# Kernel optimization log

Measured on AMD Instinct MI355X. Metric: run time of the kernel, lower is better.

Reference implementation:

```python
import jax, jax.numpy as jnp
import numpy as np

DIM = 1024
NUM_HEADS = 16
HEAD_DIM = DIM // NUM_HEADS
HIDDEN = 4 * DIM
EPS = 1e-5


def rmsnorm(x, w):
    var = jnp.mean(jnp.square(x), axis=-1, keepdims=True)
    return x * jax.lax.rsqrt(var + EPS) * w


def setup_inputs() -> dict:
    key = jax.random.key(0)
    ks = jax.random.split(key, 10)
    s = 0.02
    return {
        "x": jax.random.normal(ks[0], (2, 2048, DIM), dtype=jnp.float32),
        "wq": jax.random.normal(ks[1], (DIM, DIM), dtype=jnp.float32) * s,
        "wk": jax.random.normal(ks[2], (DIM, DIM), dtype=jnp.float32) * s,
        "wv": jax.random.normal(ks[3], (DIM, DIM), dtype=jnp.float32) * s,
        "wo": jax.random.normal(ks[4], (DIM, DIM), dtype=jnp.float32) * s,
        "wgate": jax.random.normal(ks[5], (HIDDEN, DIM), dtype=jnp.float32) * s,
        "wup": jax.random.normal(ks[6], (HIDDEN, DIM), dtype=jnp.float32) * s,
        "wdown": jax.random.normal(ks[7], (DIM, HIDDEN), dtype=jnp.float32) * s,
        "norm1_w": jnp.ones((DIM,), dtype=jnp.float32),
        "norm2_w": jnp.ones((DIM,), dtype=jnp.float32),
    }


def reference(x, wq, wk, wv, wo, wgate, wup, wdown, norm1_w, norm2_w):
    B, S, _ = x.shape
    residual = x
    h = rmsnorm(x, norm1_w)
    # torch Linear: y = x @ W.T  (W is [out, in])
    q = (h @ wq.T).reshape(B, S, NUM_HEADS, HEAD_DIM)
    k = (h @ wk.T).reshape(B, S, NUM_HEADS, HEAD_DIM)
    v = (h @ wv.T).reshape(B, S, NUM_HEADS, HEAD_DIM)
    scale = HEAD_DIM ** -0.5
    # [B, H, S, S] scores, causal mask
    scores = jnp.einsum("bqhd,bkhd->bhqk", q, k) * scale
    causal = jnp.tril(jnp.ones((S, S), dtype=bool))
    scores = jnp.where(causal, scores, -jnp.inf)
    attn = jax.nn.softmax(scores, axis=-1)
    out = jnp.einsum("bhqk,bkhd->bqhd", attn, v).reshape(B, S, DIM)
    x = residual + out @ wo.T
    residual = x
    h = rmsnorm(x, norm2_w)
    mlp = (jax.nn.silu(h @ wgate.T) * (h @ wup.T)) @ wdown.T
    return residual + mlp
```

## Files before the change

### kernel.cpp

```cpp
#include <hip/hip_runtime.h>
#include <stdint.h>

typedef __attribute__((ext_vector_type(4))) float  f32x4;
typedef __attribute__((ext_vector_type(8))) __bf16 bf16x8;
typedef __attribute__((ext_vector_type(4))) unsigned short us4;

__device__ __forceinline__ unsigned short f2bf(float f) {
  unsigned int u = __float_as_uint(f);
  unsigned int r = (u + 0x7fffu + ((u >> 16) & 1u)) >> 16;
  return (unsigned short)r;
}
__device__ __forceinline__ float bf2f(unsigned short h) {
  return __uint_as_float(((unsigned int)h) << 16);
}
__device__ __forceinline__ void gload16(const void* g, void* l) {
  __builtin_amdgcn_global_load_lds((const __attribute__((address_space(1))) void*)g,
                                   (__attribute__((address_space(3))) void*)l, 16, 0, 0);
}

__global__ __launch_bounds__(256) void convert_w(
    const float* __restrict__ wq, const float* __restrict__ wk, const float* __restrict__ wv,
    const float* __restrict__ wo, const float* __restrict__ wg, const float* __restrict__ wu,
    const float* __restrict__ wd, unsigned short* __restrict__ dst)
{
  long vid = (long)blockIdx.x * 256 + threadIdx.x;
  long e = vid * 4;
  const float* s; long base;
  if (e < (1L << 22)) { int wi = (int)(e >> 20); s = wi == 0 ? wq : wi == 1 ? wk : wi == 2 ? wv : wo; base = (long)wi << 20; }
  else if (e < (2L << 22)) { s = wg; base = 1L << 22; }
  else if (e < (3L << 22)) { s = wu; base = 2L << 22; }
  else                     { s = wd; base = 3L << 22; }
  f32x4 v = *(const f32x4*)(s + (e - base));
  us4 o; o.x = f2bf(v.x); o.y = f2bf(v.y); o.z = f2bf(v.z); o.w = f2bf(v.w);
  *(us4*)(dst + e) = o;
}

__global__ __launch_bounds__(256) void rmsnorm_k(const float* __restrict__ x,
                                                 const float* __restrict__ w,
                                                 unsigned short* __restrict__ h)
{
  const int row = blockIdx.x, t = threadIdx.x;
  const float* xr = x + (long)row * 1024;
  f32x4 v = *(const f32x4*)(xr + t * 4);
  float ss = v.x * v.x + v.y * v.y + v.z * v.z + v.w * v.w;
  #pragma unroll
  for (int o = 32; o > 0; o >>= 1) ss += __shfl_xor(ss, o);
  __shared__ float red[4];
  if ((t & 63) == 0) red[t >> 6] = ss;
  __syncthreads();
  ss = red[0] + red[1] + red[2] + red[3];
  float sc = rsqrtf(ss * (1.0f / 1024.0f) + 1e-5f);
  f32x4 wv = *(const f32x4*)(w + t * 4);
  us4 o4;
  o4.x = f2bf(v.x * sc * wv.x);
  o4.y = f2bf(v.y * sc * wv.y);
  o4.z = f2bf(v.z * sc * wv.z);
  o4.w = f2bf(v.w * sc * wv.w);
  *(us4*)(h + (long)row * 1024 + t * 4) = o4;
}

template<int EPI, int BM>
__global__ __launch_bounds__(256) void gemm_bt(
    const unsigned short* __restrict__ A, const unsigned short* __restrict__ B,
    int M, int N, int K, void* __restrict__ out0,
    const float* __restrict__ resid, const unsigned short* __restrict__ gbuf)
{
  constexpr int MI = (BM == 128) ? 4 : 2;
  __shared__ __align__(16) unsigned short Al[BM * 64];
  __shared__ __align__(16) unsigned short Bl[128 * 64];
  const int t = threadIdx.x;
  const int lane = t & 63;
  const int wid = t >> 6;
  const int wr = wid >> 1, wc = wid & 1;
  const long m0 = (long)blockIdx.x * BM;
  const long n0 = (long)blockIdx.y * 128;
  const int lr = lane & 15, lk = (lane >> 4) * 8;
  f32x4 acc[MI][4] = {};
  const int trow = t >> 3, tcol = (t & 7) * 8;
  const unsigned short* Ag = A + (m0 + trow) * (long)K + tcol;
  const unsigned short* Bg = B + (n0 + trow) * (long)K + tcol;
  unsigned short* Ald = Al + trow * 64 + tcol;
  unsigned short* Bld = Bl + trow * 64 + tcol;
  const int nkt = K >> 6;
  for (int kt = 0; kt < nkt; ++kt) {
    #pragma unroll
    for (int i = 0; i < BM / 32; ++i)
      gload16(Ag + (long)kt * 64 + (long)i * 32 * K, Ald + i * 2048);
    #pragma unroll
    for (int i = 0; i < 4; ++i)
      gload16(Bg + (long)kt * 64 + (long)i * 32 * K, Bld + i * 2048);
    __syncthreads();
    #pragma unroll
    for (int kk = 0; kk < 64; kk += 32) {
      bf16x8 af[MI], bfr[4];
      #pragma unroll
      for (int mi = 0; mi < MI; ++mi)
        af[mi] = *(const bf16x8*)&Al[(wr * (MI * 16) + mi * 16 + lr) * 64 + kk + lk];
      #pragma unroll
      for (int ni = 0; ni < 4; ++ni)
        bfr[ni] = *(const bf16x8*)&Bl[(wc * 64 + ni * 16 + lr) * 64 + kk + lk];
      #pragma unroll
      for (int mi = 0; mi < MI; ++mi)
        #pragma unroll
        for (int ni = 0; ni < 4; ++ni)
          acc[mi][ni] = __builtin_amdgcn_mfma_f32_16x16x32_bf16(af[mi], bfr[ni], acc[mi][ni], 0, 0, 0);
    }
    __syncthreads();
  }
  const int lg = lane >> 4;
  #pragma unroll
  for (int mi = 0; mi < MI; ++mi)
    #pragma unroll
    for (int ni = 0; ni < 4; ++ni)
      #pragma unroll
      for (int j = 0; j < 4; ++j) {
        long row = m0 + wr * (MI * 16) + mi * 16 + lg * 4 + j;
        long col = n0 + wc * 64 + ni * 16 + lr;
        float v = acc[mi][ni][j];
        if (EPI == 0) {
          unsigned short* qkv = (unsigned short*)out0;
          long b = row >> 11, s = row & 2047;
          if (col < 1024) {
            long hh = col >> 6, d = col & 63;
            qkv[((b * 16 + hh) * 2048 + s) * 64 + d] = f2bf(v);
          } else if (col < 2048) {
            long c = col - 1024, hh = c >> 6, d = c & 63;
            qkv[4194304 + ((b * 16 + hh) * 2048 + s) * 64 + d] = f2bf(v);
          } else {
            long c = col - 2048, hh = c >> 6, d = c & 63;
            qkv[8388608 + ((b * 16 + hh) * 64 + d) * 2048 + s] = f2bf(v);
          }
        } else if (EPI == 1) {
          ((float*)out0)[row * N + col] = resid[row * N + col] + v;
        }
      }
}

template<int EPI>
__global__ __launch_bounds__(512, 2) void gemm8(
    const unsigned short* __restrict__ A, const unsigned short* __restrict__ B,
    int M, int N, int K, unsigned short* __restrict__ out0,
    const unsigned short* __restrict__ gbuf)
{
  __shared__ __align__(16) unsigned short Asl[2][2][8192];
  __shared__ __align__(16) unsigned short Bsl[2][2][8192];
  const int t = threadIdx.x;
  const int lane = t & 63, w = t >> 6;
  const int wr = w >> 2, wc = w & 3;
  const int lr = lane & 15, lg = lane >> 4;
  const int nwg = gridDim.x * gridDim.y;
  int lid = blockIdx.y * gridDim.x + blockIdx.x;
  if ((nwg & 7) == 0) lid = (lid & 7) * (nwg >> 3) + (lid >> 3);
  const long m0 = (long)(lid % gridDim.x) * 256;
  const long n0 = (long)(lid / gridDim.x) * 256;

  const int swb = ((lr >> 2) & 1) << 5;
  const int colx0 = (lg * 16) ^ swb;
  const int colx1 = (64 + lg * 16) ^ swb;

  const int scol = ((t & 7) * 8) ^ (((t >> 5) & 1) << 4);
  const int srow = t >> 3;

  auto stage = [&](int kt, int buf) {
    const long kc = (long)kt * 64 + scol;
    #pragma unroll
    for (int h = 0; h < 2; ++h)
      #pragma unroll
      for (int j = 0; j < 2; ++j) {
        const int row = h * 128 + j * 64 + srow;
        gload16(&A[(m0 + row) * (long)K + kc], &Asl[buf][h][j * 4096 + t * 8]);
        gload16(&B[(n0 + row) * (long)K + kc], &Bsl[buf][h][j * 4096 + t * 8]);
      }
  };

  f32x4 acc[8][4] = {};
  const int nkt = K >> 6;

  stage(0, 0);
  __syncthreads();

  for (int kt = 0; kt < nkt; ++kt) {
    const int p = kt & 1;
    const char* Ab = (const char*)Asl[p][wr];
    const char* Bb = (const char*)Bsl[p][wc >> 1];
    bf16x8 breg[4][2];
    #pragma unroll
    for (int ni = 0; ni < 4; ++ni) {
      const int brow = (wc & 1) * 64 + ni * 16 + lr;
      breg[ni][0] = *(const bf16x8*)(Bb + brow * 128 + colx0);
      breg[ni][1] = *(const bf16x8*)(Bb + brow * 128 + colx1);
    }
    #pragma unroll
    for (int q2 = 0; q2 < 4; ++q2) {
      bf16x8 areg[2][2];
      #pragma unroll
      for (int mi = 0; mi < 2; ++mi) {
        const int arow = q2 * 32 + mi * 16 + lr;
        areg[mi][0] = *(const bf16x8*)(Ab + arow * 128 + colx0);
        areg[mi][1] = *(const bf16x8*)(Ab + arow * 128 + colx1);
      }
      if (q2 == 0 && kt + 1 < nkt) stage(kt + 1, p ^ 1);
      __builtin_amdgcn_s_setprio(1);
      #pragma unroll
      for (int mi = 0; mi < 2; ++mi)
        #pragma unroll
        for (int ni = 0; ni < 4; ++ni) {
          acc[q2 * 2 + mi][ni] = __builtin_amdgcn_mfma_f32_16x16x32_bf16(
              areg[mi][0], breg[ni][0], acc[q2 * 2 + mi][ni], 0, 0, 0);
          acc[q2 * 2 + mi][ni] = __builtin_amdgcn_mfma_f32_16x16x32_bf16(
              areg[mi][1], breg[ni][1], acc[q2 * 2 + mi][ni], 0, 0, 0);
        }
      __builtin_amdgcn_s_setprio(0);
      if (q2 < 3) __builtin_amdgcn_s_barrier();
    }
    asm volatile("s_waitcnt vmcnt(0)" ::: "memory");
    __builtin_amdgcn_s_barrier();
    __builtin_amdgcn_sched_barrier(0);
  }

  #pragma unroll
  for (int fi = 0; fi < 8; ++fi)
    #pragma unroll
    for (int ni = 0; ni < 4; ++ni)
      #pragma unroll
      for (int j = 0; j < 4; ++j) {
        long row = m0 + wr * 128 + fi * 16 + lg * 4 + j;
        long col = n0 + wc * 64 + ni * 16 + lr;
        float v = acc[fi][ni][j];
        if (EPI == 2) {
          out0[row * N + col] = f2bf(v);
        } else {
          float g = bf2f(gbuf[row * N + col]);
          float sg = g / (1.0f + __expf(-g));
          out0[row * N + col] = f2bf(sg * v);
        }
      }
}

__global__ __launch_bounds__(256) void attn_k(
    const unsigned short* __restrict__ qb, const unsigned short* __restrict__ kb,
    const unsigned short* __restrict__ vtb, unsigned short* __restrict__ ob)
{
  __shared__ __align__(16) unsigned short Kl[2 * 4096];
  __shared__ __align__(16) unsigned short Vl[2 * 4096];
  __shared__ __align__(16) unsigned short Pl[4 * 1024];
  const int t = threadIdx.x, lane = t & 63, w = t >> 6;
  const int pid = blockIdx.x;
  const int bh = blockIdx.y;
  const int lr = lane & 15, lg = lane >> 4;
  const long kvbase = (long)bh * 2048 * 64;
  const float SC = 0.125f * 1.4426950408889634f;

  const int trow = t >> 3;
  const int csw = (((t & 7) ^ (trow & 7)) * 8);
  auto stage = [&](int buf, int kt2) {
    #pragma unroll
    for (int i = 0; i < 2; ++i) {
      gload16(&kb[kvbase + (long)(kt2 * 64 + i * 32 + trow) * 64 + csw],
              &Kl[buf * 4096 + i * 2048 + t * 8]);
      gload16(&vtb[kvbase + (long)(i * 32 + trow) * 2048 + kt2 * 64 + csw],
              &Vl[buf * 4096 + i * 2048 + t * 8]);
    }
  };
  auto swz = [](const unsigned short* base, int row, int col) -> const bf16x8* {
    int b = ((row << 7) + (col << 1)) ^ ((row & 7) << 4);
    return (const bf16x8*)((const char*)base + b);
  };

  #pragma unroll 1
  for (int pass = 0; pass < 2; ++pass) {
    const int qt = pass ? pid : (31 - pid);
    const int q0 = qt * 64;
    bf16x8 qf[2];
    #pragma unroll
    for (int kk = 0; kk < 2; ++kk)
      qf[kk] = *(const bf16x8*)&qb[kvbase + (long)(q0 + w * 16 + lr) * 64 + kk * 32 + lg * 8];
    f32x4 oacc[4] = {};
    float mi_[4], li_[4];
    #pragma unroll
    for (int j = 0; j < 4; ++j) { mi_[j] = -1e30f; li_[j] = 0.f; }

    stage(0, 0);
    __syncthreads();
    int cur = 0;
    for (int kt = 0; kt <= qt; ++kt) {
      if (kt < qt) stage(cur ^ 1, kt + 1);
      f32x4 sa[4] = {};
      #pragma unroll
      for (int kk = 0; kk < 2; ++kk)
        #pragma unroll
        for (int ni = 0; ni < 4; ++ni) {
          bf16x8 kf = *swz(&Kl[cur * 4096], ni * 16 + lr, kk * 32 + lg * 8);
          sa[ni] = __builtin_amdgcn_mfma_f32_16x16x32_bf16(qf[kk], kf, sa[ni], 0, 0, 0);
        }
      float p[4][4];
      const bool diag = (kt == qt);
      #pragma unroll
      for (int ni = 0; ni < 4; ++ni)
        #pragma unroll
        for (int j = 0; j < 4; ++j) {
          float sv = sa[ni][j] * SC;
          if (diag && (ni * 16 + lr > w * 16 + lg * 4 + j)) sv = -1e30f;
          p[ni][j] = sv;
        }
      float mx4[4];
      #pragma unroll
      for (int j = 0; j < 4; ++j) {
        float mx = fmaxf(fmaxf(p[0][j], p[1][j]), fmaxf(p[2][j], p[3][j]));
        mx = fmaxf(mx, __shfl_xor(mx, 1));
        mx = fmaxf(mx, __shfl_xor(mx, 2));
        mx = fmaxf(mx, __shfl_xor(mx, 4));
        mx = fmaxf(mx, __shfl_xor(mx, 8));
        mx4[j] = mx;
      }
      float g = fmaxf(fmaxf(mx4[0] - mi_[0], mx4[1] - mi_[1]),
                      fmaxf(mx4[2] - mi_[2], mx4[3] - mi_[3]));
      if (!__all(g <= 8.0f)) {
        #pragma unroll
        for (int j = 0; j < 4; ++j) {
          float mnew = fmaxf(mi_[j], mx4[j]);
          float a = exp2f(mi_[j] - mnew);
          mi_[j] = mnew;
          li_[j] *= a;
          #pragma unroll
          for (int f = 0; f < 4; ++f) oacc[f][j] *= a;
        }
      }
      #pragma unroll
      for (int j = 0; j < 4; ++j) {
        float rs = 0.f;
        #pragma unroll
        for (int ni = 0; ni < 4; ++ni) { float e = exp2f(p[ni][j] - mi_[j]); p[ni][j] = e; rs += e; }
        rs += __shfl_xor(rs, 1); rs += __shfl_xor(rs, 2);
        rs += __shfl_xor(rs, 4); rs += __shfl_xor(rs, 8);
        li_[j] += rs;
      }
      unsigned short* pw = &Pl[w * 1024];
      #pragma unroll
      for (int ni = 0; ni < 4; ++ni)
        #pragma unroll
        for (int j = 0; j < 4; ++j) {
          int row = lg * 4 + j, col = ni * 16 + lr;
          int b = ((row << 7) + (col << 1)) ^ ((row & 7) << 4);
          *(unsigned short*)((char*)pw + b) = f2bf(p[ni][j]);
        }
      #pragma unroll
      for (int kk = 0; kk < 2; ++kk) {
        bf16x8 pf = *swz(pw, lr, kk * 32 + lg * 8);
        #pragma unroll
        for (int f = 0; f < 4; ++f) {
          bf16x8 vf = *swz(&Vl[cur * 4096], f * 16 + lr, kk * 32 + lg * 8);
          oacc[f] = __builtin_amdgcn_mfma_f32_16x16x32_bf16(pf, vf, oacc[f], 0, 0, 0);
        }
      }
      __syncthreads();
      cur ^= 1;
    }
    const long b = bh >> 4, hh = bh & 15;
    #pragma unroll
    for (int f = 0; f < 4; ++f)
      #pragma unroll
      for (int j = 0; j < 4; ++j) {
        long s = q0 + w * 16 + lg * 4 + j;
        long c = hh * 64 + f * 16 + lr;
        ob[(b * 2048 + s) * 1024 + c] = f2bf(oacc[f][j] / li_[j]);
      }
  }
}

extern "C" void kernel_launch(void* const* d_in, const int* in_sizes, int n_in,
                              void* d_out, int out_size, void* d_ws, size_t ws_size,
                              hipStream_t stream) {
  const float* x     = (const float*)d_in[0];
  const float* wq    = (const float*)d_in[1];
  const float* wk    = (const float*)d_in[2];
  const float* wv    = (const float*)d_in[3];
  const float* wo    = (const float*)d_in[4];
  const float* wgate = (const float*)d_in[5];
  const float* wup   = (const float*)d_in[6];
  const float* wdown = (const float*)d_in[7];
  const float* n1w   = (const float*)d_in[8];
  const float* n2w   = (const float*)d_in[9];
  float* out = (float*)d_out;

  char* ws = (char*)d_ws;
  unsigned short* wbf   = (unsigned short*)ws;
  unsigned short* h_bf  = (unsigned short*)(ws + (32L << 20));
  unsigned short* qkv   = (unsigned short*)(ws + (40L << 20));
  unsigned short* attno = (unsigned short*)(ws + (64L << 20));
  float*          x2    = (float*)(ws + (72L << 20));
  unsigned short* h2    = (unsigned short*)(ws + (88L << 20));
  unsigned short* gateb = (unsigned short*)(ws + (96L << 20));

  const unsigned short* wq_bf = wbf;
  const unsigned short* wo_bf = wbf + 3L * 1048576;
  const unsigned short* wg_bf = wbf + 4194304L;
  const unsigned short* wu_bf = wbf + 8388608L;
  const unsigned short* wd_bf = wbf + 12582912L;

  convert_w<<<16384, 256, 0, stream>>>(wq, wk, wv, wo, wgate, wup, wdown, wbf);
  rmsnorm_k<<<4096, 256, 0, stream>>>(x, n1w, h_bf);
  gemm_bt<0, 128><<<dim3(32, 24), 256, 0, stream>>>(h_bf, wq_bf, 4096, 3072, 1024, qkv, nullptr, nullptr);
  attn_k<<<dim3(16, 32), 256, 0, stream>>>(qkv, qkv + 4194304, qkv + 8388608, attno);
  gemm_bt<1, 64><<<dim3(64, 8), 256, 0, stream>>>(attno, wo_bf, 4096, 1024, 1024, x2, x, nullptr);
  rmsnorm_k<<<4096, 256, 0, stream>>>(x2, n2w, h2);
  gemm8<2><<<dim3(16, 16), 512, 0, stream>>>(h2, wg_bf, 4096, 4096, 1024, gateb, nullptr);
  gemm8<3><<<dim3(16, 16), 512, 0, stream>>>(h2, wu_bf, 4096, 4096, 1024, gateb, gateb);
  gemm_bt<1, 64><<<dim3(64, 8), 256, 0, stream>>>(gateb, wd_bf, 4096, 1024, 4096, out, x2, nullptr);
}
```

Before: 448.6 us.

## Split attention KV loop across two warp groups and move QKV GEMM to gemm8

The attention kernel now runs 512 threads: two groups of four waves each process alternating KV tiles with their own double-buffered K/V shared memory. The partial softmax states (m, l, O) are then merged through shared-memory scratch before the output is written. This doubles the waves available per query tile to hide latency, at the cost of an extra merge and more shared memory. The QKV projection also moves from the 256-thread gemm_bt to the larger-tile 512-thread gemm8 with the head-scatter epilogue, and P and the output now use a hardware bf16 convert.

```diff
diff --git a/kernel.cpp b/kernel.cpp
--- a/kernel.cpp
+++ b/kernel.cpp
@@ -9,6 +9,10 @@
   unsigned int u = __float_as_uint(f);
   unsigned int r = (u + 0x7fffu + ((u >> 16) & 1u)) >> 16;
   return (unsigned short)r;
+}
+__device__ __forceinline__ unsigned short f2bf_fast(float f) {
+  __bf16 h = (__bf16)f;
+  return __builtin_bit_cast(unsigned short, h);
 }
 __device__ __forceinline__ float bf2f(unsigned short h) {
   return __uint_as_float(((unsigned int)h) << 16);
@@ -117,20 +121,7 @@
         long row = m0 + wr * (MI * 16) + mi * 16 + lg * 4 + j;
         long col = n0 + wc * 64 + ni * 16 + lr;
         float v = acc[mi][ni][j];
-        if (EPI == 0) {
-          unsigned short* qkv = (unsigned short*)out0;
-          long b = row >> 11, s = row & 2047;
-          if (col < 1024) {
-            long hh = col >> 6, d = col & 63;
-            qkv[((b * 16 + hh) * 2048 + s) * 64 + d] = f2bf(v);
-          } else if (col < 2048) {
-            long c = col - 1024, hh = c >> 6, d = c & 63;
-            qkv[4194304 + ((b * 16 + hh) * 2048 + s) * 64 + d] = f2bf(v);
-          } else {
-            long c = col - 2048, hh = c >> 6, d = c & 63;
-            qkv[8388608 + ((b * 16 + hh) * 64 + d) * 2048 + s] = f2bf(v);
-          }
-        } else if (EPI == 1) {
+        if (EPI == 1) {
           ((float*)out0)[row * N + col] = resid[row * N + col] + v;
         }
       }
@@ -227,7 +218,19 @@
         long row = m0 + wr * 128 + fi * 16 + lg * 4 + j;
         long col = n0 + wc * 64 + ni * 16 + lr;
         float v = acc[fi][ni][j];
-        if (EPI == 2) {
+        if (EPI == 0) {
+          long b = row >> 11, s = row & 2047;
+          if (col < 1024) {
+            long hh = col >> 6, d = col & 63;
+            out0[((b * 16 + hh) * 2048 + s) * 64 + d] = f2bf(v);
+          } else if (col < 2048) {
+            long c = col - 1024, hh = c >> 6, d = c & 63;
+            out0[4194304 + ((b * 16 + hh) * 2048 + s) * 64 + d] = f2bf(v);
+          } else {
+            long c = col - 2048, hh = c >> 6, d = c & 63;
+            out0[8388608 + ((b * 16 + hh) * 64 + d) * 2048 + s] = f2bf(v);
+          }
+        } else if (EPI == 2) {
           out0[row * N + col] = f2bf(v);
         } else {
           float g = bf2f(gbuf[row * N + col]);
@@ -237,35 +240,39 @@
       }
 }
 
-__global__ __launch_bounds__(256) void attn_k(
+__global__ __launch_bounds__(512) void attn_k(
     const unsigned short* __restrict__ qb, const unsigned short* __restrict__ kb,
     const unsigned short* __restrict__ vtb, unsigned short* __restrict__ ob)
 {
-  __shared__ __align__(16) unsigned short Kl[2 * 4096];
-  __shared__ __align__(16) unsigned short Vl[2 * 4096];
-  __shared__ __align__(16) unsigned short Pl[4 * 1024];
+  __shared__ __align__(16) unsigned short Kl[2][2][4096];
+  __shared__ __align__(16) unsigned short Vl[2][2][4096];
+  __shared__ __align__(16) unsigned short Pl[8][1024];
   const int t = threadIdx.x, lane = t & 63, w = t >> 6;
-  const int pid = blockIdx.x;
-  const int bh = blockIdx.y;
+  const int gw = w >> 2, wl = w & 3;
+  const int tg = t & 255;
+  const int pid = blockIdx.x, bh = blockIdx.y;
   const int lr = lane & 15, lg = lane >> 4;
   const long kvbase = (long)bh * 2048 * 64;
   const float SC = 0.125f * 1.4426950408889634f;
 
-  const int trow = t >> 3;
-  const int csw = (((t & 7) ^ (trow & 7)) * 8);
+  const int trow = tg >> 3;
+  const int csw = (((tg & 7) ^ (trow & 7)) * 8);
   auto stage = [&](int buf, int kt2) {
     #pragma unroll
     for (int i = 0; i < 2; ++i) {
       gload16(&kb[kvbase + (long)(kt2 * 64 + i * 32 + trow) * 64 + csw],
-              &Kl[buf * 4096 + i * 2048 + t * 8]);
+              &Kl[gw][buf][i * 2048 + tg * 8]);
       gload16(&vtb[kvbase + (long)(i * 32 + trow) * 2048 + kt2 * 64 + csw],
-              &Vl[buf * 4096 + i * 2048 + t * 8]);
+              &Vl[gw][buf][i * 2048 + tg * 8]);
     }
   };
   auto swz = [](const unsigned short* base, int row, int col) -> const bf16x8* {
     int b = ((row << 7) + (col << 1)) ^ ((row & 7) << 4);
     return (const bf16x8*)((const char*)base + b);
   };
+  float* Oscr = (float*)&Kl[0][0][0];
+  float* Mscr = (float*)&Vl[0][0][0];
+  float* Lscr = Mscr + 64;
 
   #pragma unroll 1
   for (int pass = 0; pass < 2; ++pass) {
@@ -274,97 +281,127 @@
     bf16x8 qf[2];
     #pragma unroll
     for (int kk = 0; kk < 2; ++kk)
-      qf[kk] = *(const bf16x8*)&qb[kvbase + (long)(q0 + w * 16 + lr) * 64 + kk * 32 + lg * 8];
+      qf[kk] = *(const bf16x8*)&qb[kvbase + (long)(q0 + wl * 16 + lr) * 64 + kk * 32 + lg * 8];
     f32x4 oacc[4] = {};
     float mi_[4], li_[4];
     #pragma unroll
     for (int j = 0; j < 4; ++j) { mi_[j] = -1e30f; li_[j] = 0.f; }
 
-    stage(0, 0);
+    if (gw <= qt) stage(0, gw);
     __syncthreads();
     int cur = 0;
-    for (int kt = 0; kt <= qt; ++kt) {
-      if (kt < qt) stage(cur ^ 1, kt + 1);
-      f32x4 sa[4] = {};
-      #pragma unroll
-      for (int kk = 0; kk < 2; ++kk)
-        #pragma unroll
-        for (int ni = 0; ni < 4; ++ni) {
-          bf16x8 kf = *swz(&Kl[cur * 4096], ni * 16 + lr, kk * 32 + lg * 8);
-          sa[ni] = __builtin_amdgcn_mfma_f32_16x16x32_bf16(qf[kk], kf, sa[ni], 0, 0, 0);
-        }
-      float p[4][4];
-      const bool diag = (kt == qt);
-      #pragma unroll
-      for (int ni = 0; ni < 4; ++ni)
+    const int niter = (qt >> 1) + 1;
+    for (int i = 0; i < niter; ++i) {
+      const int kt = gw + 2 * i;
+      const bool act = (kt <= qt);
+      if (act && kt + 2 <= qt) stage(cur ^ 1, kt + 2);
+      if (act) {
+        f32x4 sa[4] = {};
+        #pragma unroll
+        for (int kk = 0; kk < 2; ++kk)
+          #pragma unroll
+          for (int ni = 0; ni < 4; ++ni) {
+            bf16x8 kf = *swz(&Kl[gw][cur][0], ni * 16 + lr, kk * 32 + lg * 8);
+            sa[ni] = __builtin_amdgcn_mfma_f32_16x16x32_bf16(qf[kk], kf, sa[ni], 0, 0, 0);
+          }
+        float p[4][4];
+        const bool diag = (kt == qt);
+        #pragma unroll
+        for (int ni = 0; ni < 4; ++ni)
+          #pragma unroll
+          for (int j = 0; j < 4; ++j) {
+            float sv = sa[ni][j] * SC;
+            if (diag && (ni * 16 + lr > wl * 16 + lg * 4 + j)) sv = -1e30f;
+            p[ni][j] = sv;
+          }
+        float mx4[4];
         #pragma unroll
         for (int j = 0; j < 4; ++j) {
-          float sv = sa[ni][j] * SC;
-          if (diag && (ni * 16 + lr > w * 16 + lg * 4 + j)) sv = -1e30f;
-          p[ni][j] = sv;
-        }
-      float mx4[4];
-      #pragma unroll
-      for (int j = 0; j < 4; ++j) {
-        float mx = fmaxf(fmaxf(p[0][j], p[1][j]), fmaxf(p[2][j], p[3][j]));
-        mx = fmaxf(mx, __shfl_xor(mx, 1));
-        mx = fmaxf(mx, __shfl_xor(mx, 2));
-        mx = fmaxf(mx, __shfl_xor(mx, 4));
-        mx = fmaxf(mx, __shfl_xor(mx, 8));
-        mx4[j] = mx;
-      }
-      float g = fmaxf(fmaxf(mx4[0] - mi_[0], mx4[1] - mi_[1]),
-                      fmaxf(mx4[2] - mi_[2], mx4[3] - mi_[3]));
-      if (!__all(g <= 8.0f)) {
+          float mx = fmaxf(fmaxf(p[0][j], p[1][j]), fmaxf(p[2][j], p[3][j]));
+          mx = fmaxf(mx, __shfl_xor(mx, 1));
+          mx = fmaxf(mx, __shfl_xor(mx, 2));
+          mx = fmaxf(mx, __shfl_xor(mx, 4));
+          mx = fmaxf(mx, __shfl_xor(mx, 8));
+          mx4[j] = mx;
+        }
+        float g = fmaxf(fmaxf(mx4[0] - mi_[0], mx4[1] - mi_[1]),
+                        fmaxf(mx4[2] - mi_[2], mx4[3] - mi_[3]));
+        if (!__all(g <= 8.0f)) {
+          #pragma unroll
+          for (int j = 0; j < 4; ++j) {
+            float mnew = fmaxf(mi_[j], mx4[j]);
+            float a = exp2f(mi_[j] - mnew);
+            mi_[j] = mnew;
+            li_[j] *= a;
+            #pragma unroll
+            for (int f = 0; f < 4; ++f) oacc[f][j] *= a;
+          }
+        }
         #pragma unroll
         for (int j = 0; j < 4; ++j) {
-          float mnew = fmaxf(mi_[j], mx4[j]);
-          float a = exp2f(mi_[j] - mnew);
-          mi_[j] = mnew;
-          li_[j] *= a;
-          #pragma unroll
-          for (int f = 0; f < 4; ++f) oacc[f][j] *= a;
-        }
-      }
-      #pragma unroll
-      for (int j = 0; j < 4; ++j) {
-        float rs = 0.f;
-        #pragma unroll
-        for (int ni = 0; ni < 4; ++ni) { float e = exp2f(p[ni][j] - mi_[j]); p[ni][j] = e; rs += e; }
-        rs += __shfl_xor(rs, 1); rs += __shfl_xor(rs, 2);
-        rs += __shfl_xor(rs, 4); rs += __shfl_xor(rs, 8);
-        li_[j] += rs;
-      }
-      unsigned short* pw = &Pl[w * 1024];
-      #pragma unroll
-      for (int ni = 0; ni < 4; ++ni)
-        #pragma unroll
-        for (int j = 0; j < 4; ++j) {
-          int row = lg * 4 + j, col = ni * 16 + lr;
-          int b = ((row << 7) + (col << 1)) ^ ((row & 7) << 4);
-          *(unsigned short*)((char*)pw + b) = f2bf(p[ni][j]);
-        }
-      #pragma unroll
-      for (int kk = 0; kk < 2; ++kk) {
-        bf16x8 pf = *swz(pw, lr, kk * 32 + lg * 8);
-        #pragma unroll
-        for (int f = 0; f < 4; ++f) {
-          bf16x8 vf = *swz(&Vl[cur * 4096], f * 16 + lr, kk * 32 + lg * 8);
-          oacc[f] = __builtin_amdgcn_mfma_f32_16x16x32_bf16(pf, vf, oacc[f], 0, 0, 0);
+          float rs = 0.f;
+          #pragma unroll
+          for (int ni = 0; ni < 4; ++ni) { float e = exp2f(p[ni][j] - mi_[j]); p[ni][j] = e; rs += e; }
+          rs += __shfl_xor(rs, 1); rs += __shfl_xor(rs, 2);
+          rs += __shfl_xor(rs, 4); rs += __shfl_xor(rs, 8);
+          li_[j] += rs;
+        }
+        unsigned short* pw = &Pl[w][0];
+        #pragma unroll
+        for (int ni = 0; ni < 4; ++ni)
+          #pragma unroll
+          for (int j = 0; j < 4; ++j) {
+            int row = lg * 4 + j, col = ni * 16 + lr;
+            int b = ((row << 7) + (col << 1)) ^ ((row & 7) << 4);
+            *(unsigned short*)((char*)pw + b) = f2bf_fast(p[ni][j]);
+          }
+        #pragma unroll
+        for (int kk = 0; kk < 2; ++kk) {
+          bf16x8 pf = *swz(pw, lr, kk * 32 + lg * 8);
+          #pragma unroll
+          for (int f = 0; f < 4; ++f) {
+            bf16x8 vf = *swz(&Vl[gw][cur][0], f * 16 + lr, kk * 32 + lg * 8);
+            oacc[f] = __builtin_amdgcn_mfma_f32_16x16x32_bf16(pf, vf, oacc[f], 0, 0, 0);
+          }
         }
       }
       __syncthreads();
       cur ^= 1;
     }
-    const long b = bh >> 4, hh = bh & 15;
-    #pragma unroll
-    for (int f = 0; f < 4; ++f)
+    if (gw == 1) {
+      #pragma unroll
+      for (int f = 0; f < 4; ++f)
+        #pragma unroll
+        for (int j = 0; j < 4; ++j)
+          Oscr[wl * 1024 + (lg * 4 + j) * 64 + f * 16 + lr] = oacc[f][j];
+      if (lr == 0) {
+        #pragma unroll
+        for (int j = 0; j < 4; ++j) {
+          Mscr[wl * 16 + lg * 4 + j] = mi_[j];
+          Lscr[wl * 16 + lg * 4 + j] = li_[j];
+        }
+      }
+    }
+    __syncthreads();
+    if (gw == 0) {
+      const long b = bh >> 4, hh = bh & 15;
       #pragma unroll
       for (int j = 0; j < 4; ++j) {
-        long s = q0 + w * 16 + lg * 4 + j;
-        long c = hh * 64 + f * 16 + lr;
-        ob[(b * 2048 + s) * 1024 + c] = f2bf(oacc[f][j] / li_[j]);
-      }
+        float mB = Mscr[wl * 16 + lg * 4 + j];
+        float lB = Lscr[wl * 16 + lg * 4 + j];
+        float m = fmaxf(mi_[j], mB);
+        float a0 = exp2f(mi_[j] - m), a1 = exp2f(mB - m);
+        float linv = 1.0f / (li_[j] * a0 + lB * a1);
+        long s = q0 + wl * 16 + lg * 4 + j;
+        #pragma unroll
+        for (int f = 0; f < 4; ++f) {
+          float o = (oacc[f][j] * a0 +
+                     Oscr[wl * 1024 + (lg * 4 + j) * 64 + f * 16 + lr] * a1) * linv;
+          ob[(b * 2048 + s) * 1024 + hh * 64 + f * 16 + lr] = f2bf_fast(o);
+        }
+      }
+    }
+    __syncthreads();
   }
 }
 
@@ -400,8 +437,8 @@
 
   convert_w<<<16384, 256, 0, stream>>>(wq, wk, wv, wo, wgate, wup, wdown, wbf);
   rmsnorm_k<<<4096, 256, 0, stream>>>(x, n1w, h_bf);
-  gemm_bt<0, 128><<<dim3(32, 24), 256, 0, stream>>>(h_bf, wq_bf, 4096, 3072, 1024, qkv, nullptr, nullptr);
-  attn_k<<<dim3(16, 32), 256, 0, stream>>>(qkv, qkv + 4194304, qkv + 8388608, attno);
+  gemm8<0><<<dim3(16, 12), 512, 0, stream>>>(h_bf, wq_bf, 4096, 3072, 1024, qkv, nullptr);
+  attn_k<<<dim3(16, 32), 512, 0, stream>>>(qkv, qkv + 4194304, qkv + 8388608, attno);
   gemm_bt<1, 64><<<dim3(64, 8), 256, 0, stream>>>(attno, wo_bf, 4096, 1024, 1024, x2, x, nullptr);
   rmsnorm_k<<<4096, 256, 0, stream>>>(x2, n2w, h2);
   gemm8<2><<<dim3(16, 16), 512, 0, stream>>>(h2, wg_bf, 4096, 4096, 1024, gateb, nullptr);
```

Result: slower. 494.5 us (+10.2%).

## Triple-buffer K/V tiles in attention with vmcnt-based waits, use native bf16 convert

Applied to the files above, without the earlier changes.

The attention kernel moves from double to triple buffering of K/V tiles in LDS, prefetching two tiles ahead. It replaces __syncthreads with explicit s_waitcnt vmcnt plus s_barrier, so only the oldest in-flight loads have to land before each barrier. The P and output conversions now use the compiler's native bf16 cast instead of manual rounding. The change raises LDS use per block, which can lower occupancy. It also prefetches tiles past qt up to 31, which is wasted traffic on causal rows, and those stray loads are still in flight when the next pass stages buffers 0 and 1.

```diff
diff --git a/kernel.cpp b/kernel.cpp
--- a/kernel.cpp
+++ b/kernel.cpp
@@ -9,6 +9,10 @@
   unsigned int u = __float_as_uint(f);
   unsigned int r = (u + 0x7fffu + ((u >> 16) & 1u)) >> 16;
   return (unsigned short)r;
+}
+__device__ __forceinline__ unsigned short f2bf_fast(float f) {
+  __bf16 h = (__bf16)f;
+  return __builtin_bit_cast(unsigned short, h);
 }
 __device__ __forceinline__ float bf2f(unsigned short h) {
   return __uint_as_float(((unsigned int)h) << 16);
@@ -241,12 +245,11 @@
     const unsigned short* __restrict__ qb, const unsigned short* __restrict__ kb,
     const unsigned short* __restrict__ vtb, unsigned short* __restrict__ ob)
 {
-  __shared__ __align__(16) unsigned short Kl[2 * 4096];
-  __shared__ __align__(16) unsigned short Vl[2 * 4096];
+  __shared__ __align__(16) unsigned short Kl[3 * 4096];
+  __shared__ __align__(16) unsigned short Vl[3 * 4096];
   __shared__ __align__(16) unsigned short Pl[4 * 1024];
   const int t = threadIdx.x, lane = t & 63, w = t >> 6;
-  const int pid = blockIdx.x;
-  const int bh = blockIdx.y;
+  const int pid = blockIdx.x, bh = blockIdx.y;
   const int lr = lane & 15, lg = lane >> 4;
   const long kvbase = (long)bh * 2048 * 64;
   const float SC = 0.125f * 1.4426950408889634f;
@@ -281,16 +284,25 @@
     for (int j = 0; j < 4; ++j) { mi_[j] = -1e30f; li_[j] = 0.f; }
 
     stage(0, 0);
-    __syncthreads();
+    stage(1, 1);
+    asm volatile("s_waitcnt vmcnt(4)" ::: "memory");
+    __builtin_amdgcn_sched_barrier(0);
+    __builtin_amdgcn_s_barrier();
+
     int cur = 0;
     for (int kt = 0; kt <= qt; ++kt) {
-      if (kt < qt) stage(cur ^ 1, kt + 1);
+      const int nxt = kt + 2;
+      const bool dostage = (nxt <= 31);
+      const int nbuf = cur >= 1 ? cur - 1 : cur + 2;
+      if (dostage) stage(nbuf, nxt);
+      const unsigned short* Kb = &Kl[cur * 4096];
+      const unsigned short* Vb = &Vl[cur * 4096];
       f32x4 sa[4] = {};
       #pragma unroll
       for (int kk = 0; kk < 2; ++kk)
         #pragma unroll
         for (int ni = 0; ni < 4; ++ni) {
-          bf16x8 kf = *swz(&Kl[cur * 4096], ni * 16 + lr, kk * 32 + lg * 8);
+          bf16x8 kf = *swz(Kb, ni * 16 + lr, kk * 32 + lg * 8);
           sa[ni] = __builtin_amdgcn_mfma_f32_16x16x32_bf16(qf[kk], kf, sa[ni], 0, 0, 0);
         }
       float p[4][4];
@@ -342,19 +354,22 @@
         for (int j = 0; j < 4; ++j) {
           int row = lg * 4 + j, col = ni * 16 + lr;
           int b = ((row << 7) + (col << 1)) ^ ((row & 7) << 4);
-          *(unsigned short*)((char*)pw + b) = f2bf(p[ni][j]);
+          *(unsigned short*)((char*)pw + b) = f2bf_fast(p[ni][j]);
         }
       #pragma unroll
       for (int kk = 0; kk < 2; ++kk) {
         bf16x8 pf = *swz(pw, lr, kk * 32 + lg * 8);
         #pragma unroll
         for (int f = 0; f < 4; ++f) {
-          bf16x8 vf = *swz(&Vl[cur * 4096], f * 16 + lr, kk * 32 + lg * 8);
+          bf16x8 vf = *swz(Vb, f * 16 + lr, kk * 32 + lg * 8);
           oacc[f] = __builtin_amdgcn_mfma_f32_16x16x32_bf16(pf, vf, oacc[f], 0, 0, 0);
         }
       }
-      __syncthreads();
-      cur ^= 1;
+      if (dostage) { asm volatile("s_waitcnt vmcnt(4)" ::: "memory"); }
+      else         { asm volatile("s_waitcnt vmcnt(0)" ::: "memory"); }
+      __builtin_amdgcn_sched_barrier(0);
+      __builtin_amdgcn_s_barrier();
+      cur = (cur == 2) ? 0 : cur + 1;
     }
     const long b = bh >> 4, hh = bh & 15;
     #pragma unroll
@@ -363,7 +378,7 @@
       for (int j = 0; j < 4; ++j) {
         long s = q0 + w * 16 + lg * 4 + j;
         long c = hh * 64 + f * 16 + lr;
-        ob[(b * 2048 + s) * 1024 + c] = f2bf(oacc[f][j] / li_[j]);
+        ob[(b * 2048 + s) * 1024 + c] = f2bf_fast(oacc[f][j] / li_[j]);
       }
   }
 }
```

After: 448.8 us. No clear change (+0.0%).
